# Kernel optimization log

Hardware: AMD Instinct MI355X
Metric: run time of the kernel (lower is better)

Reference implementation:

```python
import jax, jax.numpy as jnp
import numpy as np

B, C, F, T = 8, 64, 256, 512
CA = 5          # channel_attention
NTHR = 23       # number of threshold channels (loop breaks at i=24 where cnt hits 1.0)
BN_EPS = 1e-5

# thresholds: cnt accumulates i*(1/300) in python float -> cnt_i = i(i+1)/600
THRESHOLDS = jnp.asarray(np.cumsum(np.arange(1, NTHR + 1) / 300.0), dtype=jnp.float32)


def setup_inputs() -> dict:
    key = jax.random.key(0)
    ks = jax.random.split(key, 12)
    s = 0.05
    return {
        "feature_in": jax.random.normal(ks[0], (B, C, F, T), jnp.float32),
        "w1": jax.random.normal(ks[1], (CA, C), jnp.float32) * s,   # cov1d_d_1 weight [out,in] (k=1)
        "b1": jax.random.normal(ks[2], (CA,), jnp.float32) * s,
        "w2": jax.random.normal(ks[3], (C, CA), jnp.float32) * s,   # cov1d_d_2 weight
        "b2": jax.random.normal(ks[4], (C,), jnp.float32) * s,
        "wc": jax.random.normal(ks[5], (C,), jnp.float32) * s,      # conv2d_fn C->1, 1x1
        "bc": jax.random.normal(ks[6], (1,), jnp.float32) * s,
        "wc2": jax.random.normal(ks[7], (C, NTHR), jnp.float32) * s,  # conv2d_fn_2 23->C, 1x1
        "bc2": jax.random.normal(ks[8], (C,), jnp.float32) * s,
        "wo": jax.random.normal(ks[9], (C, 2 * C), jnp.float32) * s,  # out_conv2d 2C->C, 1x1
        "bo": jax.random.normal(ks[10], (C,), jnp.float32) * s,
        "gamma": jnp.ones((C,), jnp.float32),
        "beta": jnp.zeros((C,), jnp.float32),
    }


def _chan_mlp(z, w1, b1, w2, b2):
    # z: [B, C, L] -> sigmoid(conv1(relu(conv0(z)))) ; both convs are kernel-1 channel mixes
    h = jax.nn.relu(jnp.einsum('oc,bcl->bol', w1, z) + b1[None, :, None])
    return jax.nn.sigmoid(jnp.einsum('co,bol->bcl', w2, h) + b2[None, :, None])


def reference(feature_in, w1, b1, w2, b2, wc, bc, wc2, bc2, wo, bo, gamma, beta):
    # --- DTFA ---
    zt = _chan_mlp(jnp.mean(feature_in, axis=2), w1, b1, w2, b2)  # [B,C,T]
    zf = _chan_mlp(jnp.mean(feature_in, axis=3), w1, b1, w2, b2)  # [B,C,F]
    # matmul([B,C,F,1],[B,C,1,T]) == outer-product broadcast
    outer = zf[:, :, :, None] * zt[:, :, None, :]                 # [B,C,F,T]
    att_map = jnp.einsum('bcft,c->bft', outer, wc) + bc[0]        # [B,F,T] (squeezed 1-channel)
    # thresholded channel stack: channel i = att_map * (att_map > thr_i)
    dcomp = jnp.where(att_map[:, None] > THRESHOLDS[None, :, None, None],
                      att_map[:, None], 0.0)                      # [B,23,F,T]
    att = jnp.einsum('bkft,ck->bcft', dcomp, wc2) + bc2[None, :, None, None]
    att = att * feature_in                                        # [B,C,F,T]
    # --- block tail: concat -> 1x1 conv -> BN(train stats) -> ReLU ---
    concat = jnp.concatenate([feature_in, att], axis=1)           # [B,2C,F,T]
    o = jnp.einsum('bkft,ck->bcft', concat, wo) + bo[None, :, None, None]
    mu = jnp.mean(o, axis=(0, 2, 3), keepdims=True)
    var = jnp.var(o, axis=(0, 2, 3), keepdims=True)
    o = (o - mu) * jax.lax.rsqrt(var + BN_EPS)
    o = o * gamma[None, :, None, None] + beta[None, :, None, None]
    return jax.nn.relu(o)
```

## Files before the change

kernel.cpp:

```cpp
#include <hip/hip_runtime.h>

#define Bn 8
#define Cn 64
#define Fn 256
#define Tn 512
#define FT (Fn*Tn)
#define NPIX (Bn*Fn*Tn)
#define NTOT (Bn*Cn*Fn*Tn)

#define WS_MT    0
#define WS_MF    262144
#define WS_ZT    393216
#define WS_ZFW   655360
#define WS_P     786432
#define WS_THR   787968
#define WS_AHI   788000
#define WS_ALO   792096
#define WS_PSH   796192
#define WS_SCALE 804384
#define WS_SHIFT 804448

typedef __attribute__((ext_vector_type(8))) short bf16x8;
typedef __attribute__((ext_vector_type(4))) float f32x4;

__device__ __forceinline__ void split2(float x, unsigned short& h, unsigned short& l) {
    unsigned u = __builtin_bit_cast(unsigned, x);
    unsigned r = u + 0x7FFFu + ((u >> 16) & 1u);
    h = (unsigned short)(r >> 16);
    float hf = __builtin_bit_cast(float, r & 0xFFFF0000u);
    float lo = x - hf;
    unsigned ul = __builtin_bit_cast(unsigned, lo);
    unsigned rl = ul + 0x7FFFu + ((ul >> 16) & 1u);
    l = (unsigned short)(rl >> 16);
}

__device__ __forceinline__ unsigned pk2(float a, float b) {
    unsigned r;
    asm("v_cvt_pk_bf16_f32 %0, %1, %2" : "=v"(r) : "v"(a), "v"(b));
    return r;
}

__global__ __launch_bounds__(256) void k1_sums(const float* __restrict__ x,
                                               float* __restrict__ ws) {
    const int bx = blockIdx.x;
    const int slab = bx >> 3, chunk = bx & 7;
    const int wave = threadIdx.x >> 6, lane = threadIdx.x & 63;
    const float4* x4 = (const float4*)x + (size_t)slab * (FT / 4) + chunk * 32 * 128;
    __shared__ float lcs[4 * 512];
    float4 cs0 = {0.f,0.f,0.f,0.f}, cs1 = {0.f,0.f,0.f,0.f};
    #pragma unroll
    for (int r = 0; r < 8; ++r) {
        const int row = wave * 8 + r;
        float4 v0 = x4[row * 128 + lane];
        float4 v1 = x4[row * 128 + 64 + lane];
        cs0.x += v0.x; cs0.y += v0.y; cs0.z += v0.z; cs0.w += v0.w;
        cs1.x += v1.x; cs1.y += v1.y; cs1.z += v1.z; cs1.w += v1.w;
        float rs = (v0.x + v0.y) + (v0.z + v0.w) + (v1.x + v1.y) + (v1.z + v1.w);
        #pragma unroll
        for (int m = 1; m < 64; m <<= 1) rs += __shfl_xor(rs, m, 64);
        if (lane == 0) ws[WS_MF + slab * Fn + chunk * 32 + row] = rs;
    }
    ((float4*)lcs)[wave * 128 + lane] = cs0;
    ((float4*)lcs)[wave * 128 + 64 + lane] = cs1;
    __syncthreads();
    for (int t = threadIdx.x; t < 512; t += 256) {
        float s = lcs[t] + lcs[512 + t] + lcs[1024 + t] + lcs[1536 + t];
        atomicAdd(&ws[WS_MT + slab * Tn + t], s);
    }
}

__global__ __launch_bounds__(256) void k2_mlp_prep(
    const float* __restrict__ w1, const float* __restrict__ b1,
    const float* __restrict__ w2, const float* __restrict__ b2,
    const float* __restrict__ wc, const float* __restrict__ bc2,
    const float* __restrict__ wo, const float* __restrict__ wc2,
    float* __restrict__ ws) {
    const int blk = blockIdx.x;
    if (blk < 1536) {
        const int wave = threadIdx.x >> 6, c = threadIdx.x & 63;
        const bool is_t = (blk < 1024);
        float m; int b, l;
        if (is_t) {
            const int p = blk * 4 + wave;
            b = p >> 9; l = p & 511;
            m = ws[WS_MT + (b * 64 + c) * Tn + l] * (1.0f / Fn);
        } else {
            const int p = (blk - 1024) * 4 + wave;
            b = p >> 8; l = p & 255;
            m = ws[WS_MF + (b * 64 + c) * Fn + l] * (1.0f / Tn);
        }
        float acc = b2[c];
        #pragma unroll
        for (int o = 0; o < 5; ++o) {
            float v = w1[o * 64 + c] * m;
            #pragma unroll
            for (int mm = 1; mm < 64; mm <<= 1) v += __shfl_xor(v, mm, 64);
            const float h = fmaxf(v + b1[o], 0.0f);
            acc = fmaf(w2[c * 5 + o], h, acc);
        }
        const float sg = 1.0f / (1.0f + expf(-acc));
        if (is_t) ws[WS_ZT  + (b * 64 + c) * Tn + l] = sg;
        else      ws[WS_ZFW + (b * 64 + c) * Fn + l] = sg * wc[c];
    } else {
        const int tid = threadIdx.x;
        unsigned short* AH = (unsigned short*)(ws + WS_AHI);
        unsigned short* AL = (unsigned short*)(ws + WS_ALO);
        for (int i = tid; i < 8192; i += 256) {
            const int chunk = i >> 9, within = i & 511;
            const int quad = within >> 7, m16 = (within >> 3) & 15, j = within & 7;
            const int m = (chunk & 3) * 16 + m16;
            const int k = (chunk >> 2) * 32 + quad * 8 + j;
            float v;
            if (k < 64) v = wo[m * 128 + k] + wo[m * 128 + 64 + k] * bc2[k];
            else        v = wo[m * 128 + k];
            unsigned short h, l;
            split2(v, h, l);
            AH[i] = h; AL[i] = l;
        }
        for (int c = tid; c < 64; c += 256) {
            float a = 0.f;
            ws[WS_P + c * 24 + 0] = 0.f;
            for (int K = 1; K <= 23; ++K) { a += wc2[c * 23 + K - 1]; ws[WS_P + c * 24 + K] = a; }
        }
        if (tid == 0) {
            double a = 0.0;
            for (int i = 1; i <= 23; ++i) { a += (double)i / 300.0; ws[WS_THR + i - 1] = (float)a; }
            for (int i = 23; i < 32; ++i) ws[WS_THR + i] = 1e30f;
        }
        for (int i = tid; i < 8192; i += 256) ws[WS_PSH + i] = 0.f;
    }
}

__global__ __launch_bounds__(256, 5) void k4_main(
    const float* __restrict__ x, const float* __restrict__ wsc,
    const float* __restrict__ bc, const float* __restrict__ bo,
    float* __restrict__ out, float* __restrict__ ws) {
    __shared__ __align__(16) short Bhi[16 * 512];
    __shared__ __align__(16) short Blo[8 * 512];
    __shared__ float Pl[64 * 24];
    __shared__ float AmP[4 * 64];
    __shared__ float sstat[128];

    const int tid = threadIdx.x;
    const int blk = blockIdx.x;
    const int b = blk >> 11;
    const int rem = blk & 2047;
    const int f = rem >> 3;
    const int t0 = (rem & 7) << 6;

    const int t_local = tid & 63, kg = tid >> 6;
    const int t = t0 + t_local;
    const int nfrag = t_local >> 4, n16 = t_local & 15;

    const float* xb = x + (size_t)b * (Cn * FT) + f * Tn + t;
    float xv[16];
    #pragma unroll
    for (int g = 0; g < 2; ++g) {
        const int k8 = (kg + g * 4) << 3;
        #pragma unroll
        for (int i = 0; i < 8; ++i) xv[g * 8 + i] = xb[(size_t)(k8 + i) * FT];
    }

    for (int i = tid; i < 1536; i += 256) Pl[i] = wsc[WS_P + i];

    const float* zfw = wsc + WS_ZFW + b * (Cn * Fn) + f;
    const float* zt  = wsc + WS_ZT  + b * (Cn * Tn) + t;
    float amp = 0.f;
    #pragma unroll
    for (int cc = 0; cc < 16; ++cc) {
        const int c = kg * 16 + cc;
        amp = fmaf(zfw[c * Fn], zt[c * Tn], amp);
    }
    AmP[kg * 64 + t_local] = amp;

    #pragma unroll
    for (int g = 0; g < 2; ++g) {
        const int k8 = (kg + g * 4) << 3;
        unsigned ph[4], pl[4];
        #pragma unroll
        for (int i = 0; i < 4; ++i) {
            const float x0 = xv[g * 8 + 2 * i], x1 = xv[g * 8 + 2 * i + 1];
            const unsigned h = pk2(x0, x1);
            const float hf0 = __builtin_bit_cast(float, h << 16);
            const float hf1 = __builtin_bit_cast(float, h & 0xFFFF0000u);
            ph[i] = h;
            pl[i] = pk2(x0 - hf0, x1 - hf1);
        }
        const int cka = ((k8 >> 5) * 4 + nfrag) * 512 + ((k8 >> 3) & 3) * 128 + n16 * 8;
        *(int4*)&Bhi[cka] = make_int4(ph[0], ph[1], ph[2], ph[3]);
        *(int4*)&Blo[cka] = make_int4(pl[0], pl[1], pl[2], pl[3]);
    }
    __syncthreads();

    float am = bc[0] + AmP[t_local] + AmP[64 + t_local] + AmP[128 + t_local] + AmP[192 + t_local];
    int L = 0;
    #pragma unroll
    for (int i = 0; i < 23; ++i) L += (am > wsc[WS_THR + i]) ? 1 : 0;

    #pragma unroll
    for (int g = 0; g < 2; ++g) {
        const int k8 = (kg + g * 4) << 3;
        unsigned pg[4];
        #pragma unroll
        for (int i = 0; i < 4; ++i) {
            const float g0 = am * Pl[(k8 + 2 * i)     * 24 + L] * xv[g * 8 + 2 * i];
            const float g1 = am * Pl[(k8 + 2 * i + 1) * 24 + L] * xv[g * 8 + 2 * i + 1];
            pg[i] = pk2(g0, g1);
        }
        const int cka = ((k8 >> 5) * 4 + nfrag) * 512 + ((k8 >> 3) & 3) * 128 + n16 * 8;
        *(int4*)&Bhi[cka + 4096] = make_int4(pg[0], pg[1], pg[2], pg[3]);
    }
    __syncthreads();

    const int lane = tid & 63, w = tid >> 6;
    const int quad = lane >> 4, l16 = lane & 15;
    const short* AH = (const short*)(wsc + WS_AHI);
    const short* AL = (const short*)(wsc + WS_ALO);

    f32x4 acc[4];
    const float4 bo4 = *(const float4*)&bo[w * 16 + quad * 4];
    #pragma unroll
    for (int nf = 0; nf < 4; ++nf) { acc[nf].x = bo4.x; acc[nf].y = bo4.y; acc[nf].z = bo4.z; acc[nf].w = bo4.w; }

    #pragma unroll
    for (int ks = 0; ks < 4; ++ks) {
        const int ao = (ks * 4 + w) * 512 + quad * 128 + l16 * 8;
        const bf16x8 ah = *(const bf16x8*)(AH + ao);
        const bf16x8 al = *(const bf16x8*)(AL + ao);
        #pragma unroll
        for (int nf = 0; nf < 4; ++nf) {
            const int bof = (ks * 4 + nf) * 512 + quad * 128 + l16 * 8;
            const bf16x8 bh = *(const bf16x8*)&Bhi[bof];
            acc[nf] = __builtin_amdgcn_mfma_f32_16x16x32_bf16(ah, bh, acc[nf], 0, 0, 0);
            if (ks < 2) {
                const bf16x8 bl = *(const bf16x8*)&Blo[bof];
                acc[nf] = __builtin_amdgcn_mfma_f32_16x16x32_bf16(ah, bl, acc[nf], 0, 0, 0);
            }
            acc[nf] = __builtin_amdgcn_mfma_f32_16x16x32_bf16(al, bh, acc[nf], 0, 0, 0);
        }
    }

    float* ob = out + (size_t)b * (Cn * FT) + f * Tn + t0;
    #pragma unroll
    for (int r = 0; r < 4; ++r) {
        const int c = w * 16 + quad * 4 + r;
        float vs = 0.f, vq = 0.f;
        #pragma unroll
        for (int nf = 0; nf < 4; ++nf) {
            const float v = acc[nf][r];
            ob[(size_t)c * FT + nf * 16 + l16] = v;
            vs += v; vq = fmaf(v, v, vq);
        }
        #pragma unroll
        for (int m = 1; m < 16; m <<= 1) { vs += __shfl_xor(vs, m); vq += __shfl_xor(vq, m); }
        if (l16 == 0) { sstat[c] = vs; sstat[64 + c] = vq; }
    }
    __syncthreads();
    if (tid < 128) atomicAdd(&ws[WS_PSH + (blk & 63) * 128 + tid], sstat[tid]);
}

__global__ __launch_bounds__(256) void k7_norm(float* __restrict__ o,
                                               const float* __restrict__ gamma,
                                               const float* __restrict__ beta,
                                               const float* __restrict__ ws) {
    __shared__ float ssc[64], ssh[64];
    const int tid = threadIdx.x;
    if (tid < 64) {
        float s = 0.f, q = 0.f;
        #pragma unroll 8
        for (int sh = 0; sh < 64; ++sh) {
            s += ws[WS_PSH + sh * 128 + tid];
            q += ws[WS_PSH + sh * 128 + 64 + tid];
        }
        const float n = (float)NPIX;
        const float mu = s / n;
        const float var = q / n - mu * mu;
        const float sc = gamma[tid] * rsqrtf(var + 1e-5f);
        ssc[tid] = sc;
        ssh[tid] = beta[tid] - mu * sc;
    }
    __syncthreads();
    const int blk = blockIdx.x;
    const int slab = blk >> 5, chunk = blk & 31;
    const int c = slab & 63;
    const float sc = ssc[c], sh = ssh[c];
    float4* o4 = (float4*)o + (size_t)slab * (FT / 4) + chunk * 1024;
    #pragma unroll
    for (int i = 0; i < 4; ++i) {
        float4 v = o4[i * 256 + tid];
        v.x = fmaxf(fmaf(v.x, sc, sh), 0.f);
        v.y = fmaxf(fmaf(v.y, sc, sh), 0.f);
        v.z = fmaxf(fmaf(v.z, sc, sh), 0.f);
        v.w = fmaxf(fmaf(v.w, sc, sh), 0.f);
        o4[i * 256 + tid] = v;
    }
}

extern "C" void kernel_launch(void* const* d_in, const int* in_sizes, int n_in,
                              void* d_out, int out_size, void* d_ws, size_t ws_size,
                              hipStream_t stream) {
    const float* x     = (const float*)d_in[0];
    const float* w1    = (const float*)d_in[1];
    const float* b1    = (const float*)d_in[2];
    const float* w2    = (const float*)d_in[3];
    const float* b2    = (const float*)d_in[4];
    const float* wc    = (const float*)d_in[5];
    const float* bc    = (const float*)d_in[6];
    const float* wc2   = (const float*)d_in[7];
    const float* bc2   = (const float*)d_in[8];
    const float* wo    = (const float*)d_in[9];
    const float* bo    = (const float*)d_in[10];
    const float* gamma = (const float*)d_in[11];
    const float* beta  = (const float*)d_in[12];
    float* out = (float*)d_out;
    float* ws  = (float*)d_ws;

    hipMemsetAsync(ws + WS_MT, 0, Bn * Cn * Tn * sizeof(float), stream);
    k1_sums<<<4096, 256, 0, stream>>>(x, ws);
    k2_mlp_prep<<<1537, 256, 0, stream>>>(w1, b1, w2, b2, wc, bc2, wo, wc2, ws);
    k4_main<<<16384, 256, 0, stream>>>(x, ws, bc, bo, out, ws);
    k7_norm<<<16384, 256, 0, stream>>>(out, gamma, beta, ws);
}
```

Before: 686.2 us.

## Process two T-tiles per block with prefetch and transposed z layouts

Each k4_main block now handles 128 time steps as two 64-wide tiles, so half as many blocks are launched. The second tile's x and zt loads are issued before the first tile's MFMA and epilogue to overlap memory latency with compute. zt and zfw are stored channel-contiguous so each thread reads them with float4 vector loads instead of strided scalar loads. Per-block setup (Pl copy, zf, bias) is amortised over two tiles, and BN partial stats are accumulated across both tiles before one atomic. In exchange, register pressure rises (launch bounds lowered from 5 to 4) and parallelism is reduced.

New measurement: 707.2 us. 1.03x slower.

```diff
diff --git a/kernel.cpp b/kernel.cpp
--- a/kernel.cpp
+++ b/kernel.cpp
@@ -99,8 +99,8 @@
             acc = fmaf(w2[c * 5 + o], h, acc);
         }
         const float sg = 1.0f / (1.0f + expf(-acc));
-        if (is_t) ws[WS_ZT  + (b * 64 + c) * Tn + l] = sg;
-        else      ws[WS_ZFW + (b * 64 + c) * Fn + l] = sg * wc[c];
+        if (is_t) ws[WS_ZT  + ((b * Tn + l) << 6) + c] = sg;
+        else      ws[WS_ZFW + ((b * Fn + l) << 6) + c] = sg * wc[c];
     } else {
         const int tid = threadIdx.x;
         unsigned short* AH = (unsigned short*)(ws + WS_AHI);
@@ -131,129 +131,170 @@
     }
 }
 
-__global__ __launch_bounds__(256, 5) void k4_main(
+#define XSTAGE(XV, ZT)  do {                                                      \
+    float amp = 0.f;                                                              \
+    _Pragma("unroll")                                                             \
+    for (int q = 0; q < 4; ++q) {                                                 \
+      amp = fmaf(zf[q].x, ZT[q].x, amp);                                          \
+      amp = fmaf(zf[q].y, ZT[q].y, amp);                                          \
+      amp = fmaf(zf[q].z, ZT[q].z, amp);                                          \
+      amp = fmaf(zf[q].w, ZT[q].w, amp);                                          \
+    }                                                                             \
+    AmP[kg * 64 + t_local] = amp;                                                 \
+    _Pragma("unroll")                                                             \
+    for (int g = 0; g < 2; ++g) {                                                 \
+      const int k8 = (kg + g * 4) << 3;                                           \
+      unsigned ph[4], pl[4];                                                      \
+      _Pragma("unroll")                                                           \
+      for (int i = 0; i < 4; ++i) {                                               \
+        const float x0 = XV[g * 8 + 2 * i], x1 = XV[g * 8 + 2 * i + 1];           \
+        const unsigned h = pk2(x0, x1);                                           \
+        const float hf0 = __builtin_bit_cast(float, h << 16);                     \
+        const float hf1 = __builtin_bit_cast(float, h & 0xFFFF0000u);             \
+        ph[i] = h;                                                                \
+        pl[i] = pk2(x0 - hf0, x1 - hf1);                  \
+      }                                                                           \
+      const int cka = ((k8 >> 5) * 4 + nfrag) * 512 + ((k8 >> 3) & 3) * 128 + n16 * 8; \
+      *(int4*)&Bhi[cka] = make_int4(ph[0], ph[1], ph[2], ph[3]);                  \
+      *(int4*)&Blo[cka] = make_int4(pl[0], pl[1], pl[2], pl[3]);                  \
+    }                                                                             \
+  } while (0)
+
+#define GSTAGE(XV)  do {                                                          \
+    float am = bc0 + AmP[t_local] + AmP[64 + t_local] + AmP[128 + t_local] + AmP[192 + t_local]; \
+    int L = 0;                                                                    \
+    _Pragma("unroll")                                                             \
+    for (int i = 0; i < 23; ++i) L += (am > wsc[WS_THR + i]) ? 1 : 0;             \
+    _Pragma("unroll")                                                             \
+    for (int g = 0; g < 2; ++g) {                                                 \
+      const int k8 = (kg + g * 4) << 3;                                           \
+      unsigned pg[4];                                                             \
+      _Pragma("unroll")                                                           \
+      for (int i = 0; i < 4; ++i) {                                               \
+        const float g0 = am * Pl[(k8 + 2 * i)     * 24 + L] * XV[g * 8 + 2 * i];  \
+        const float g1 = am * Pl[(k8 + 2 * i + 1) * 24 + L] * XV[g * 8 + 2 * i + 1]; \
+        pg[i] = pk2(g0, g1);                                                      \
+      }                                                                           \
+      const int cka = ((k8 >> 5) * 4 + nfrag) * 512 + ((k8 >> 3) & 3) * 128 + n16 * 8; \
+      *(int4*)&Bhi[cka + 4096] = make_int4(pg[0], pg[1], pg[2], pg[3]);           \
+    }                                                                             \
+  } while (0)
+
+#define MFMA_EPI(TOFF)  do {                                                      \
+    f32x4 acc[4];                                                                 \
+    _Pragma("unroll")                                                             \
+    for (int nf = 0; nf < 4; ++nf) { acc[nf].x = bo4.x; acc[nf].y = bo4.y; acc[nf].z = bo4.z; acc[nf].w = bo4.w; } \
+    _Pragma("unroll")                                                             \
+    for (int ks = 0; ks < 4; ++ks) {                                              \
+      const int ao = (ks * 4 + w) * 512 + quad * 128 + l16 * 8;                   \
+      const bf16x8 ah = *(const bf16x8*)(AH + ao);                                \
+      const bf16x8 al = *(const bf16x8*)(AL + ao);                                \
+      _Pragma("unroll")                                                           \
+      for (int nf = 0; nf < 4; ++nf) {                                            \
+        const int bof = (ks * 4 + nf) * 512 + quad * 128 + l16 * 8;               \
+        const bf16x8 bh = *(const bf16x8*)&Bhi[bof];                              \
+        acc[nf] = __builtin_amdgcn_mfma_f32_16x16x32_bf16(ah, bh, acc[nf], 0, 0, 0); \
+        if (ks < 2) {                   \
+          const bf16x8 bl = *(const bf16x8*)&Blo[bof];                            \
+          acc[nf] = __builtin_amdgcn_mfma_f32_16x16x32_bf16(ah, bl, acc[nf], 0, 0, 0); \
+        }                                                                         \
+        acc[nf] = __builtin_amdgcn_mfma_f32_16x16x32_bf16(al, bh, acc[nf], 0, 0, 0); \
+      }                                                                           \
+    }                                                                             \
+    float* ob = out + (size_t)b * (Cn * FT) + f * Tn + t0 + (TOFF);               \
+    _Pragma("unroll")                                                             \
+    for (int r = 0; r < 4; ++r) {                                                 \
+      const int c = w * 16 + quad * 4 + r;                                        \
+      float vs = 0.f, vq = 0.f;                                                   \
+      _Pragma("unroll")                                                           \
+      for (int nf = 0; nf < 4; ++nf) {                                            \
+        const float v = acc[nf][r];                                               \
+        ob[(size_t)c * FT + nf * 16 + l16] = v;                                   \
+        vs += v; vq = fmaf(v, v, vq);                                             \
+      }                                                                           \
+      vsA[r] += vs; vqA[r] += vq;                                                 \
+    }                                                                             \
+  } while (0)
+
+__global__ __launch_bounds__(256, 4) void k4_main(
     const float* __restrict__ x, const float* __restrict__ wsc,
     const float* __restrict__ bc, const float* __restrict__ bo,
     float* __restrict__ out, float* __restrict__ ws) {
     __shared__ __align__(16) short Bhi[16 * 512];
     __shared__ __align__(16) short Blo[8 * 512];
     __shared__ float Pl[64 * 24];
-    __shared__ float AmP[4 * 64];
+    __shared__ float AmP[256];
     __shared__ float sstat[128];
 
     const int tid = threadIdx.x;
     const int blk = blockIdx.x;
-    const int b = blk >> 11;
-    const int rem = blk & 2047;
-    const int f = rem >> 3;
-    const int t0 = (rem & 7) << 6;
+    const int b = blk >> 10;
+    const int rem = blk & 1023;
+    const int f = rem >> 2;
+    const int t0 = (rem & 3) << 7;
 
     const int t_local = tid & 63, kg = tid >> 6;
-    const int t = t0 + t_local;
     const int nfrag = t_local >> 4, n16 = t_local & 15;
-
-    const float* xb = x + (size_t)b * (Cn * FT) + f * Tn + t;
-    float xv[16];
-    #pragma unroll
-    for (int g = 0; g < 2; ++g) {
-        const int k8 = (kg + g * 4) << 3;
-        #pragma unroll
-        for (int i = 0; i < 8; ++i) xv[g * 8 + i] = xb[(size_t)(k8 + i) * FT];
-    }
-
+    const int w = kg, quad = nfrag, l16 = n16;
+
+    float xv0[16]; float4 zt0[4];
+    {
+        const float* xb = x + (size_t)b * (Cn * FT) + f * Tn + t0 + t_local;
+        #pragma unroll
+        for (int g = 0; g < 2; ++g) {
+            const int k8 = (kg + g * 4) << 3;
+            #pragma unroll
+            for (int i = 0; i < 8; ++i) xv0[g * 8 + i] = xb[(size_t)(k8 + i) * FT];
+        }
+        const float4* ztp = (const float4*)(wsc + WS_ZT + ((b * Tn + t0 + t_local) << 6)) + kg * 4;
+        #pragma unroll
+        for (int q = 0; q < 4; ++q) zt0[q] = ztp[q];
+    }
+    float4 zf[4];
+    {
+        const float4* zfp = (const float4*)(wsc + WS_ZFW + ((b * Fn + f) << 6)) + kg * 4;
+        #pragma unroll
+        for (int q = 0; q < 4; ++q) zf[q] = zfp[q];
+    }
     for (int i = tid; i < 1536; i += 256) Pl[i] = wsc[WS_P + i];
-
-    const float* zfw = wsc + WS_ZFW + b * (Cn * Fn) + f;
-    const float* zt  = wsc + WS_ZT  + b * (Cn * Tn) + t;
-    float amp = 0.f;
-    #pragma unroll
-    for (int cc = 0; cc < 16; ++cc) {
-        const int c = kg * 16 + cc;
-        amp = fmaf(zfw[c * Fn], zt[c * Tn], amp);
-    }
-    AmP[kg * 64 + t_local] = amp;
-
-    #pragma unroll
-    for (int g = 0; g < 2; ++g) {
-        const int k8 = (kg + g * 4) << 3;
-        unsigned ph[4], pl[4];
-        #pragma unroll
-        for (int i = 0; i < 4; ++i) {
-            const float x0 = xv[g * 8 + 2 * i], x1 = xv[g * 8 + 2 * i + 1];
-            const unsigned h = pk2(x0, x1);
-            const float hf0 = __builtin_bit_cast(float, h << 16);
-            const float hf1 = __builtin_bit_cast(float, h & 0xFFFF0000u);
-            ph[i] = h;
-            pl[i] = pk2(x0 - hf0, x1 - hf1);
-        }
-        const int cka = ((k8 >> 5) * 4 + nfrag) * 512 + ((k8 >> 3) & 3) * 128 + n16 * 8;
-        *(int4*)&Bhi[cka] = make_int4(ph[0], ph[1], ph[2], ph[3]);
-        *(int4*)&Blo[cka] = make_int4(pl[0], pl[1], pl[2], pl[3]);
-    }
-    __syncthreads();
-
-    float am = bc[0] + AmP[t_local] + AmP[64 + t_local] + AmP[128 + t_local] + AmP[192 + t_local];
-    int L = 0;
-    #pragma unroll
-    for (int i = 0; i < 23; ++i) L += (am > wsc[WS_THR + i]) ? 1 : 0;
-
-    #pragma unroll
-    for (int g = 0; g < 2; ++g) {
-        const int k8 = (kg + g * 4) << 3;
-        unsigned pg[4];
-        #pragma unroll
-        for (int i = 0; i < 4; ++i) {
-            const float g0 = am * Pl[(k8 + 2 * i)     * 24 + L] * xv[g * 8 + 2 * i];
-            const float g1 = am * Pl[(k8 + 2 * i + 1) * 24 + L] * xv[g * 8 + 2 * i + 1];
-            pg[i] = pk2(g0, g1);
-        }
-        const int cka = ((k8 >> 5) * 4 + nfrag) * 512 + ((k8 >> 3) & 3) * 128 + n16 * 8;
-        *(int4*)&Bhi[cka + 4096] = make_int4(pg[0], pg[1], pg[2], pg[3]);
-    }
-    __syncthreads();
-
-    const int lane = tid & 63, w = tid >> 6;
-    const int quad = lane >> 4, l16 = lane & 15;
+    const float bc0 = bc[0];
+    const float4 bo4 = *(const float4*)&bo[w * 16 + quad * 4];
     const short* AH = (const short*)(wsc + WS_AHI);
     const short* AL = (const short*)(wsc + WS_ALO);
-
-    f32x4 acc[4];
-    const float4 bo4 = *(const float4*)&bo[w * 16 + quad * 4];
-    #pragma unroll
-    for (int nf = 0; nf < 4; ++nf) { acc[nf].x = bo4.x; acc[nf].y = bo4.y; acc[nf].z = bo4.z; acc[nf].w = bo4.w; }
-
-    #pragma unroll
-    for (int ks = 0; ks < 4; ++ks) {
-        const int ao = (ks * 4 + w) * 512 + quad * 128 + l16 * 8;
-        const bf16x8 ah = *(const bf16x8*)(AH + ao);
-        const bf16x8 al = *(const bf16x8*)(AL + ao);
-        #pragma unroll
-        for (int nf = 0; nf < 4; ++nf) {
-            const int bof = (ks * 4 + nf) * 512 + quad * 128 + l16 * 8;
-            const bf16x8 bh = *(const bf16x8*)&Bhi[bof];
-            acc[nf] = __builtin_amdgcn_mfma_f32_16x16x32_bf16(ah, bh, acc[nf], 0, 0, 0);
-            if (ks < 2) {
-                const bf16x8 bl = *(const bf16x8*)&Blo[bof];
-                acc[nf] = __builtin_amdgcn_mfma_f32_16x16x32_bf16(ah, bl, acc[nf], 0, 0, 0);
-            }
-            acc[nf] = __builtin_amdgcn_mfma_f32_16x16x32_bf16(al, bh, acc[nf], 0, 0, 0);
-        }
-    }
-
-    float* ob = out + (size_t)b * (Cn * FT) + f * Tn + t0;
+    float vsA[4] = {0.f,0.f,0.f,0.f}, vqA[4] = {0.f,0.f,0.f,0.f};
+
+    XSTAGE(xv0, zt0);
+    __syncthreads();
+    GSTAGE(xv0);
+    __syncthreads();
+    float xv1[16]; float4 zt1[4];
+    {
+        const float* xb = x + (size_t)b * (Cn * FT) + f * Tn + t0 + 64 + t_local;
+        #pragma unroll
+        for (int g = 0; g < 2; ++g) {
+            const int k8 = (kg + g * 4) << 3;
+            #pragma unroll
+            for (int i = 0; i < 8; ++i) xv1[g * 8 + i] = xb[(size_t)(k8 + i) * FT];
+        }
+        const float4* ztp = (const float4*)(wsc + WS_ZT + ((b * Tn + t0 + 64 + t_local) << 6)) + kg * 4;
+        #pragma unroll
+        for (int q = 0; q < 4; ++q) zt1[q] = ztp[q];
+    }
+    MFMA_EPI(0);
+    __syncthreads();
+
+    XSTAGE(xv1, zt1);
+    __syncthreads();
+    GSTAGE(xv1);
+    __syncthreads();
+    MFMA_EPI(64);
+
     #pragma unroll
     for (int r = 0; r < 4; ++r) {
-        const int c = w * 16 + quad * 4 + r;
-        float vs = 0.f, vq = 0.f;
-        #pragma unroll
-        for (int nf = 0; nf < 4; ++nf) {
-            const float v = acc[nf][r];
-            ob[(size_t)c * FT + nf * 16 + l16] = v;
-            vs += v; vq = fmaf(v, v, vq);
-        }
+        float vs = vsA[r], vq = vqA[r];
         #pragma unroll
         for (int m = 1; m < 16; m <<= 1) { vs += __shfl_xor(vs, m); vq += __shfl_xor(vq, m); }
-        if (l16 == 0) { sstat[c] = vs; sstat[64 + c] = vq; }
+        if (l16 == 0) { const int c = w * 16 + quad * 4 + r; sstat[c] = vs; sstat[64 + c] = vq; }
     }
     __syncthreads();
     if (tid < 128) atomicAdd(&ws[WS_PSH + (blk & 63) * 128 + tid], sstat[tid]);
@@ -318,6 +359,6 @@
     hipMemsetAsync(ws + WS_MT, 0, Bn * Cn * Tn * sizeof(float), stream);
     k1_sums<<<4096, 256, 0, stream>>>(x, ws);
     k2_mlp_prep<<<1537, 256, 0, stream>>>(w1, b1, w2, b2, wc, bc2, wo, wc2, ws);
-    k4_main<<<16384, 256, 0, stream>>>(x, ws, bc, bo, out, ws);
+    k4_main<<<8192, 256, 0, stream>>>(x, ws, bc, bo, out, ws);
     k7_norm<<<16384, 256, 0, stream>>>(out, gamma, beta, ws);
 }
```

## Store pre-norm output as fp16, drop x low-part MFMA, transpose z layouts

Applied to the files above, without the earlier changes.

The main kernel now writes the pre-BatchNorm activations to an fp16 workspace buffer instead of fp32 output, and the norm kernel reads fp16 and writes fp32. This halves the intermediate write and read traffic. The bf16 low-part correction for x (the Blo buffer and its extra MFMAs) is removed, and zt/zf are stored channel-innermost so each thread can load them as float4 vectors. Occupancy hint rises from 5 to 6. These changes lower accuracy (bf16-only x, fp16 intermediate) and may push error toward tolerance.

New measurement: 660.2 us. 1.04x faster.

```diff
diff --git a/kernel.cpp b/kernel.cpp
--- a/kernel.cpp
+++ b/kernel.cpp
@@ -17,11 +17,11 @@
 #define WS_AHI   788000
 #define WS_ALO   792096
 #define WS_PSH   796192
-#define WS_SCALE 804384
-#define WS_SHIFT 804448
+#define WS_O16   805888
 
 typedef __attribute__((ext_vector_type(8))) short bf16x8;
 typedef __attribute__((ext_vector_type(4))) float f32x4;
+typedef __attribute__((ext_vector_type(4))) _Float16 f16x4;
 
 __device__ __forceinline__ void split2(float x, unsigned short& h, unsigned short& l) {
     unsigned u = __builtin_bit_cast(unsigned, x);
@@ -99,8 +99,8 @@
             acc = fmaf(w2[c * 5 + o], h, acc);
         }
         const float sg = 1.0f / (1.0f + expf(-acc));
-        if (is_t) ws[WS_ZT  + (b * 64 + c) * Tn + l] = sg;
-        else      ws[WS_ZFW + (b * 64 + c) * Fn + l] = sg * wc[c];
+        if (is_t) ws[WS_ZT  + ((b * Tn + l) << 6) + c] = sg;
+        else      ws[WS_ZFW + ((b * Fn + l) << 6) + c] = sg * wc[c];
     } else {
         const int tid = threadIdx.x;
         unsigned short* AH = (unsigned short*)(ws + WS_AHI);
@@ -131,14 +131,13 @@
     }
 }
 
-__global__ __launch_bounds__(256, 5) void k4_main(
+__global__ __launch_bounds__(256, 6) void k4_main(
     const float* __restrict__ x, const float* __restrict__ wsc,
     const float* __restrict__ bc, const float* __restrict__ bo,
-    float* __restrict__ out, float* __restrict__ ws) {
+    float* __restrict__ ws) {
     __shared__ __align__(16) short Bhi[16 * 512];
-    __shared__ __align__(16) short Blo[8 * 512];
     __shared__ float Pl[64 * 24];
-    __shared__ float AmP[4 * 64];
+    __shared__ float AmP[256];
     __shared__ float sstat[128];
 
     const int tid = threadIdx.x;
@@ -149,10 +148,9 @@
     const int t0 = (rem & 7) << 6;
 
     const int t_local = tid & 63, kg = tid >> 6;
-    const int t = t0 + t_local;
     const int nfrag = t_local >> 4, n16 = t_local & 15;
 
-    const float* xb = x + (size_t)b * (Cn * FT) + f * Tn + t;
+    const float* xb = x + (size_t)b * (Cn * FT) + f * Tn + t0 + t_local;
     float xv[16];
     #pragma unroll
     for (int g = 0; g < 2; ++g) {
@@ -160,39 +158,37 @@
         #pragma unroll
         for (int i = 0; i < 8; ++i) xv[g * 8 + i] = xb[(size_t)(k8 + i) * FT];
     }
-
+    float4 zt[4], zf[4];
+    {
+        const float4* ztp = (const float4*)(wsc + WS_ZT  + ((size_t)(b * Tn + t0 + t_local) << 6)) + kg * 4;
+        const float4* zfp = (const float4*)(wsc + WS_ZFW + ((size_t)(b * Fn + f) << 6)) + kg * 4;
+        #pragma unroll
+        for (int q = 0; q < 4; ++q) { zt[q] = ztp[q]; zf[q] = zfp[q]; }
+    }
     for (int i = tid; i < 1536; i += 256) Pl[i] = wsc[WS_P + i];
 
-    const float* zfw = wsc + WS_ZFW + b * (Cn * Fn) + f;
-    const float* zt  = wsc + WS_ZT  + b * (Cn * Tn) + t;
     float amp = 0.f;
     #pragma unroll
-    for (int cc = 0; cc < 16; ++cc) {
-        const int c = kg * 16 + cc;
-        amp = fmaf(zfw[c * Fn], zt[c * Tn], amp);
+    for (int q = 0; q < 4; ++q) {
+        amp = fmaf(zf[q].x, zt[q].x, amp);
+        amp = fmaf(zf[q].y, zt[q].y, amp);
+        amp = fmaf(zf[q].z, zt[q].z, amp);
+        amp = fmaf(zf[q].w, zt[q].w, amp);
     }
     AmP[kg * 64 + t_local] = amp;
 
     #pragma unroll
     for (int g = 0; g < 2; ++g) {
         const int k8 = (kg + g * 4) << 3;
-        unsigned ph[4], pl[4];
-        #pragma unroll
-        for (int i = 0; i < 4; ++i) {
-            const float x0 = xv[g * 8 + 2 * i], x1 = xv[g * 8 + 2 * i + 1];
-            const unsigned h = pk2(x0, x1);
-            const float hf0 = __builtin_bit_cast(float, h << 16);
-            const float hf1 = __builtin_bit_cast(float, h & 0xFFFF0000u);
-            ph[i] = h;
-            pl[i] = pk2(x0 - hf0, x1 - hf1);
-        }
+        unsigned ph[4];
+        #pragma unroll
+        for (int i = 0; i < 4; ++i) ph[i] = pk2(xv[g * 8 + 2 * i], xv[g * 8 + 2 * i + 1]);
         const int cka = ((k8 >> 5) * 4 + nfrag) * 512 + ((k8 >> 3) & 3) * 128 + n16 * 8;
         *(int4*)&Bhi[cka] = make_int4(ph[0], ph[1], ph[2], ph[3]);
-        *(int4*)&Blo[cka] = make_int4(pl[0], pl[1], pl[2], pl[3]);
-    }
-    __syncthreads();
-
-    float am = bc[0] + AmP[t_local] + AmP[64 + t_local] + AmP[128 + t_local] + AmP[192 + t_local];
+    }
+    __syncthreads();
+
+    const float am = bc[0] + AmP[t_local] + AmP[64 + t_local] + AmP[128 + t_local] + AmP[192 + t_local];
     int L = 0;
     #pragma unroll
     for (int i = 0; i < 23; ++i) L += (am > wsc[WS_THR + i]) ? 1 : 0;
@@ -212,8 +208,7 @@
     }
     __syncthreads();
 
-    const int lane = tid & 63, w = tid >> 6;
-    const int quad = lane >> 4, l16 = lane & 15;
+    const int w = kg, quad = nfrag, l16 = n16;
     const short* AH = (const short*)(wsc + WS_AHI);
     const short* AL = (const short*)(wsc + WS_ALO);
 
@@ -232,15 +227,11 @@
             const int bof = (ks * 4 + nf) * 512 + quad * 128 + l16 * 8;
             const bf16x8 bh = *(const bf16x8*)&Bhi[bof];
             acc[nf] = __builtin_amdgcn_mfma_f32_16x16x32_bf16(ah, bh, acc[nf], 0, 0, 0);
-            if (ks < 2) {
-                const bf16x8 bl = *(const bf16x8*)&Blo[bof];
-                acc[nf] = __builtin_amdgcn_mfma_f32_16x16x32_bf16(ah, bl, acc[nf], 0, 0, 0);
-            }
             acc[nf] = __builtin_amdgcn_mfma_f32_16x16x32_bf16(al, bh, acc[nf], 0, 0, 0);
         }
     }
 
-    float* ob = out + (size_t)b * (Cn * FT) + f * Tn + t0;
+    _Float16* ob = (_Float16*)(ws + WS_O16) + (size_t)b * (Cn * FT) + f * Tn + t0;
     #pragma unroll
     for (int r = 0; r < 4; ++r) {
         const int c = w * 16 + quad * 4 + r;
@@ -248,7 +239,7 @@
         #pragma unroll
         for (int nf = 0; nf < 4; ++nf) {
             const float v = acc[nf][r];
-            ob[(size_t)c * FT + nf * 16 + l16] = v;
+            ob[(size_t)c * FT + nf * 16 + l16] = (_Float16)v;
             vs += v; vq = fmaf(v, v, vq);
         }
         #pragma unroll
@@ -259,7 +250,7 @@
     if (tid < 128) atomicAdd(&ws[WS_PSH + (blk & 63) * 128 + tid], sstat[tid]);
 }
 
-__global__ __launch_bounds__(256) void k7_norm(float* __restrict__ o,
+__global__ __launch_bounds__(256) void k7_norm(float* __restrict__ out,
                                                const float* __restrict__ gamma,
                                                const float* __restrict__ beta,
                                                const float* __restrict__ ws) {
@@ -284,15 +275,17 @@
     const int slab = blk >> 5, chunk = blk & 31;
     const int c = slab & 63;
     const float sc = ssc[c], sh = ssh[c];
-    float4* o4 = (float4*)o + (size_t)slab * (FT / 4) + chunk * 1024;
+    const _Float16* ip = (const _Float16*)(ws + WS_O16) + (size_t)slab * FT + chunk * 4096;
+    float4* op = (float4*)(out + (size_t)slab * FT + chunk * 4096);
     #pragma unroll
     for (int i = 0; i < 4; ++i) {
-        float4 v = o4[i * 256 + tid];
-        v.x = fmaxf(fmaf(v.x, sc, sh), 0.f);
-        v.y = fmaxf(fmaf(v.y, sc, sh), 0.f);
-        v.z = fmaxf(fmaf(v.z, sc, sh), 0.f);
-        v.w = fmaxf(fmaf(v.w, sc, sh), 0.f);
-        o4[i * 256 + tid] = v;
+        f16x4 h = *(const f16x4*)(ip + i * 1024 + tid * 4);
+        float4 v;
+        v.x = fmaxf(fmaf((float)h[0], sc, sh), 0.f);
+        v.y = fmaxf(fmaf((float)h[1], sc, sh), 0.f);
+        v.z = fmaxf(fmaf((float)h[2], sc, sh), 0.f);
+        v.w = fmaxf(fmaf((float)h[3], sc, sh), 0.f);
+        op[i * 256 + tid] = v;
     }
 }
 
@@ -318,6 +311,6 @@
     hipMemsetAsync(ws + WS_MT, 0, Bn * Cn * Tn * sizeof(float), stream);
     k1_sums<<<4096, 256, 0, stream>>>(x, ws);
     k2_mlp_prep<<<1537, 256, 0, stream>>>(w1, b1, w2, b2, wc, bc2, wo, wc2, ws);
-    k4_main<<<16384, 256, 0, stream>>>(x, ws, bc, bo, out, ws);
+    k4_main<<<16384, 256, 0, stream>>>(x, ws, bc, bo, ws);
     k7_norm<<<16384, 256, 0, stream>>>(out, gamma, beta, ws);
 }
```
